# Kernel tuning notes

Hardware: AMD Instinct MI355X
Metric: run time of the kernel (lower is better)

Reference implementation:

```python
import jax, jax.numpy as jnp
import numpy as np

N = 50000
F = 128
E = 800000
HOP = 3
ALPHA = 0.2  # leaky relu slope


def setup_inputs() -> dict:
    key = jax.random.key(0)
    ks = jax.random.split(key, 6)
    x = jax.random.normal(ks[0], (N, F), dtype=jnp.float32)
    h0 = jax.random.normal(ks[1], (N, F), dtype=jnp.float32)
    edge_index = jax.random.randint(ks[2], (2, E), 0, N, dtype=jnp.int32)
    edge_weight = jax.random.uniform(ks[3], (E,), dtype=jnp.float32)
    # xavier-uniform-ish params
    lim_w = float(np.sqrt(6.0 / (F + F)))
    W_att = jax.random.uniform(ks[4], (F, F), dtype=jnp.float32, minval=-lim_w, maxval=lim_w)
    lim_a = 1.414 * float(np.sqrt(6.0 / (2 * F + 1)))
    a = jax.random.uniform(ks[5], (2 * F, 1), dtype=jnp.float32, minval=-lim_a, maxval=lim_a)
    temp = jnp.zeros((4,), dtype=jnp.float32)
    return {"x": x, "h0": h0, "edge_index": edge_index, "edge_weight": edge_weight,
            "W_att": W_att, "a": a, "temp": temp}


def _segment_softmax(e, rows, num_segments):
    m = jax.ops.segment_max(e, rows, num_segments=num_segments)
    m = jnp.where(jnp.isfinite(m), m, 0.0)  # guard empty rows
    ex = jnp.exp(e - m[rows])
    s = jax.ops.segment_sum(ex, rows, num_segments=num_segments)
    s = jnp.where(s > 0, s, 1.0)
    return ex / s[rows]


def reference(x, h0, edge_index, edge_weight, W_att, a, temp):
    rows, cols = edge_index[0], edge_index[1]
    # --- attention (edge-wise, never materializing dense NxN e) ---
    feat = x @ W_att                       # [N, F]
    f1 = (feat @ a[:F]).squeeze(-1)        # [N]
    f2 = (feat @ a[F:]).squeeze(-1)        # [N]
    e = f1[rows] + f2[cols]                # e[i,j] at edges
    e = jnp.where(e > 0, e, ALPHA * e)     # leaky relu
    att = _segment_softmax(e, rows, N)     # sparse row softmax values
    P = 0.5 * att
    # --- lifting bases ---
    coe = jax.nn.sigmoid(temp)
    rowsum = jax.ops.segment_sum(edge_weight * P, rows, num_segments=N)  # [N]
    update = x
    feat_prime = None
    for step in range(HOP):
        # sparse mm: U @ update
        update = jax.ops.segment_sum(att[:, None] * update[cols], rows, num_segments=N)
        feat_even = coe[0] * x + update
        feat_odd = update - feat_even * rowsum[:, None]
        feat_prime = feat_odd if step == 0 else coe[2] * feat_prime + (1.0 - coe[2]) * feat_odd
    return feat_prime
```

## Files before the change

kernel.cpp:

```cpp
#include <hip/hip_runtime.h>
#include <hip/hip_fp16.h>

#define NN 50000
#define FF 128
#define EE 800000
#define ALPHA 0.2f
#define ESHIFT 4.0f

#define NBINS 196
#define CAPB 5120
#define EPB 2048
#define NWIN 784
#define WCAP 1600

__global__ void k_w(const float* __restrict__ W, const float* __restrict__ a,
                    float* __restrict__ w12) {
    int k = threadIdx.x;
    float s1 = 0.f, s2 = 0.f;
    const float* wr = W + k * FF;
    for (int j = 0; j < FF; ++j) {
        float w = wr[j];
        s1 += w * a[j];
        s2 += w * a[FF + j];
    }
    w12[k] = s1;
    w12[FF + k] = s2;
}

__global__ void k_f(const float* __restrict__ x, const float* __restrict__ w12,
                    float* __restrict__ f1, float* __restrict__ f2,
                    __half* __restrict__ xh) {
    int gid = blockIdx.x * blockDim.x + threadIdx.x;
    int node = gid >> 6;
    int lane = threadIdx.x & 63;
    if (node >= NN) return;
    float2 xv = ((const float2*)(x + (size_t)node * FF))[lane];
    ((__half2*)(xh + (size_t)node * FF))[lane] = __float22half2_rn(xv);
    float2 w1 = ((const float2*)w12)[lane];
    float2 w2 = ((const float2*)(w12 + FF))[lane];
    float s1 = xv.x * w1.x + xv.y * w1.y;
    float s2 = xv.x * w2.x + xv.y * w2.y;
#pragma unroll
    for (int o = 32; o > 0; o >>= 1) {
        s1 += __shfl_down(s1, o);
        s2 += __shfl_down(s2, o);
    }
    if (lane == 0) { f1[node] = s1; f2[node] = s2; }
}

__global__ void k_bin(const int* __restrict__ rows, const int* __restrict__ cols,
                      const float* __restrict__ ew, const float* __restrict__ f1,
                      const float* __restrict__ f2, int* __restrict__ bin_fill,
                      int2* __restrict__ binbuf) {
    __shared__ int cnt[NBINS];
    __shared__ int gbase[NBINS];
    int tid = threadIdx.x;
    if (tid < NBINS) cnt[tid] = 0;
    __syncthreads();
    int e0 = blockIdx.x * EPB;
    int rk[8], bn[8], rc[8], pay[8];
    bool vl[8];
#pragma unroll
    for (int k = 0; k < 8; ++k) {
        int e = e0 + k * 256 + tid;
        vl[k] = e < EE;
        if (vl[k]) {
            int r = rows[e], c = cols[e];
            float v = f1[r] + f2[c];
            v = v > 0.f ? v : ALPHA * v;
            float ex = __expf(v - ESHIFT);
            union { int i; __half2 h; } p;
            p.h = __floats2half2_rn(ex, ew[e] * ex);
            pay[k] = p.i;
            rc[k] = (r << 16) | c;
            bn[k] = r >> 8;
            rk[k] = atomicAdd(&cnt[bn[k]], 1);
        }
    }
    __syncthreads();
    if (tid < NBINS) {
        int c0 = cnt[tid];
        gbase[tid] = c0 ? atomicAdd(&bin_fill[tid], c0) : 0;
    }
    __syncthreads();
#pragma unroll
    for (int k = 0; k < 8; ++k) {
        if (vl[k]) {
            int pos = gbase[bn[k]] + rk[k];
            if (pos < CAPB) binbuf[(size_t)bn[k] * CAPB + pos] = make_int2(rc[k], pay[k]);
        }
    }
}

__global__ void k_csr(const int* __restrict__ bin_fill, const int2* __restrict__ binbuf,
                      int2* __restrict__ csr, int2* __restrict__ rowinfo) {
    __shared__ int lfill[64];
    __shared__ int pbase[65];
    __shared__ int cursor[64];
    int tid = threadIdx.x;
    int w = blockIdx.x;
    int bin = w >> 2, q = w & 3;
    int cnt = bin_fill[bin];
    if (cnt > CAPB) cnt = CAPB;
    if (tid < 64) lfill[tid] = 0;
    __syncthreads();
    const int2* bb = binbuf + (size_t)bin * CAPB;
    for (int i = tid; i < cnt; i += 256) {
        int rl = (bb[i].x >> 16) & 0xFF;
        if ((rl >> 6) == q) atomicAdd(&lfill[rl & 63], 1);
    }
    __syncthreads();
    if (tid < 64) {
        int pc = (lfill[tid] + 3) & ~3;
        int s = pc;
#pragma unroll
        for (int o = 1; o < 64; o <<= 1) {
            int t = __shfl_up(s, o);
            if (tid >= o) s += t;
        }
        pbase[tid + 1] = s;
        if (tid == 0) pbase[0] = 0;
    }
    __syncthreads();
    int wbase = w * WCAP;
    if (tid < 64) cursor[tid] = wbase + pbase[tid];
    __syncthreads();
    for (int i = tid; i < cnt; i += 256) {
        int2 e = bb[i];
        int rl = (e.x >> 16) & 0xFF;
        if ((rl >> 6) == q) {
            int p = atomicAdd(&cursor[rl & 63], 1);
            csr[p] = make_int2(e.x & 0xFFFF, e.y);
        }
    }
    __syncthreads();
    if (tid < 64) {
        int r = (bin << 8) + (q << 6) + tid;
        if (r < NN) {
            int beg = wbase + pbase[tid];
            int dreal = lfill[tid];
            int dpad = (dreal + 3) & ~3;
            for (int t = dreal; t < dpad; ++t) csr[beg + t] = make_int2(0, 0);
            rowinfo[r] = make_int2(beg, dpad);
        }
    }
}

__global__ void k_hop(const float* __restrict__ x, const __half* __restrict__ uin,
                      __half* __restrict__ uout, const int2* __restrict__ rowinfo,
                      const int2* __restrict__ csr, const float* __restrict__ temp,
                      __half* __restrict__ S, float* __restrict__ out, int step) {
    int wave = threadIdx.x >> 6;
    int lane = threadIdx.x & 63;
    int r = __builtin_amdgcn_readfirstlane(blockIdx.x * 4 + wave);
    if (r >= NN) return;
    int2 ri = rowinfo[r];
    const unsigned long long* bk = (const unsigned long long*)(csr + ri.x);
    int d = ri.y;
    int s = lane >> 4;
    int fl = lane & 15;
    float ax[8];
#pragma unroll
    for (int k = 0; k < 8; ++k) ax[k] = 0.f;
    float se = 0.f, sw = 0.f;
    int j = 0;
    for (; j + 16 <= d; j += 16) {
        unsigned long long b[4];
        uint4 h[4];
#pragma unroll
        for (int g = 0; g < 4; ++g)
            b[g] = __builtin_nontemporal_load(bk + j + 4 * g + s);
#pragma unroll
        for (int g = 0; g < 4; ++g) {
            int col = (int)(unsigned)(b[g] & 0xFFFFFFFFull);
            h[g] = ((const uint4*)(uin + (size_t)col * FF))[fl];
        }
#pragma unroll
        for (int g = 0; g < 4; ++g) {
            union { unsigned u; __half2 h2; } p;
            p.u = (unsigned)(b[g] >> 32);
            float2 ee = __half22float2(p.h2);
            se += ee.x;
            sw += ee.y;
            const __half2* hh = (const __half2*)&h[g];
#pragma unroll
            for (int t = 0; t < 4; ++t) {
                float2 u2 = __half22float2(hh[t]);
                ax[2 * t] += ee.x * u2.x;
                ax[2 * t + 1] += ee.x * u2.y;
            }
        }
    }
    for (; j < d; j += 4) {
        unsigned long long b = __builtin_nontemporal_load(bk + j + s);
        int col = (int)(unsigned)(b & 0xFFFFFFFFull);
        uint4 h = ((const uint4*)(uin + (size_t)col * FF))[fl];
        union { unsigned u; __half2 h2; } p;
        p.u = (unsigned)(b >> 32);
        float2 ee = __half22float2(p.h2);
        se += ee.x;
        sw += ee.y;
        const __half2* hh = (const __half2*)&h;
#pragma unroll
        for (int t = 0; t < 4; ++t) {
            float2 u2 = __half22float2(hh[t]);
            ax[2 * t] += ee.x * u2.x;
            ax[2 * t + 1] += ee.x * u2.y;
        }
    }
#pragma unroll
    for (int o = 16; o < 64; o <<= 1) {
#pragma unroll
        for (int k = 0; k < 8; ++k) ax[k] += __shfl_xor(ax[k], o);
        se += __shfl_xor(se, o);
        sw += __shfl_xor(sw, o);
    }
    float inv = se > 0.f ? 1.f / se : 0.f;
#pragma unroll
    for (int k = 0; k < 8; ++k) ax[k] *= inv;
    float c2 = 1.f / (1.f + __expf(-temp[2]));
    uint4* Sr = (uint4*)(S + (size_t)r * FF);
    if (step == 0) {
        if (s == 0) {
            union { uint4 u; __half2 h2[4]; } o1, o2;
            float w0 = c2 * c2;
#pragma unroll
            for (int t = 0; t < 4; ++t) {
                o1.h2[t] = __floats2half2_rn(ax[2 * t], ax[2 * t + 1]);
                o2.h2[t] = __floats2half2_rn(w0 * ax[2 * t], w0 * ax[2 * t + 1]);
            }
            ((uint4*)(uout + (size_t)r * FF))[fl] = o1.u;
            Sr[fl] = o2.u;
        }
    } else if (step == 1) {
        if (s == 0) {
            float w1 = c2 * (1.f - c2);
            union { uint4 u; __half2 h2[4]; } o1, sv;
            sv.u = Sr[fl];
#pragma unroll
            for (int t = 0; t < 4; ++t) {
                o1.h2[t] = __floats2half2_rn(ax[2 * t], ax[2 * t + 1]);
                float2 svf = __half22float2(sv.h2[t]);
                sv.h2[t] = __floats2half2_rn(svf.x + w1 * ax[2 * t],
                                             svf.y + w1 * ax[2 * t + 1]);
            }
            ((uint4*)(uout + (size_t)r * FF))[fl] = o1.u;
            Sr[fl] = sv.u;
        }
    } else {
        if (s == 0) {
            float rs = 0.5f * sw * inv;
            float coe0 = 1.f / (1.f + __expf(-temp[0]));
            float w2 = 1.f - c2;
            float k1 = 1.f - rs, k2 = coe0 * rs;
            union { uint4 u; __half2 h2[4]; } sv;
            sv.u = Sr[fl];
            const float4* xr = (const float4*)(x + (size_t)r * FF);
            float4* orow = (float4*)(out + (size_t)r * FF);
            float4 xv0 = xr[2 * fl], xv1 = xr[2 * fl + 1];
            float res[8];
#pragma unroll
            for (int t = 0; t < 4; ++t) {
                float2 svf = __half22float2(sv.h2[t]);
                res[2 * t] = k1 * (svf.x + w2 * ax[2 * t]);
                res[2 * t + 1] = k1 * (svf.y + w2 * ax[2 * t + 1]);
            }
            orow[2 * fl] = make_float4(res[0] - k2 * xv0.x, res[1] - k2 * xv0.y,
                                       res[2] - k2 * xv0.z, res[3] - k2 * xv0.w);
            orow[2 * fl + 1] = make_float4(res[4] - k2 * xv1.x, res[5] - k2 * xv1.y,
                                           res[6] - k2 * xv1.z, res[7] - k2 * xv1.w);
        }
    }
}

extern "C" void kernel_launch(void* const* d_in, const int* in_sizes, int n_in,
                              void* d_out, int out_size, void* d_ws, size_t ws_size,
                              hipStream_t stream) {
    const float* x = (const float*)d_in[0];
    const int* eidx = (const int*)d_in[2];
    const int* rows = eidx;
    const int* cols = eidx + EE;
    const float* ew = (const float*)d_in[3];
    const float* W = (const float*)d_in[4];
    const float* a = (const float*)d_in[5];
    const float* temp = (const float*)d_in[6];
    float* out = (float*)d_out;

    float* ws = (float*)d_ws;
    int* bin_fill = (int*)ws;
    float* w12 = ws + 256;
    float* f1 = ws + 512;
    float* f2 = f1 + NN;
    int2* rowinfo = (int2*)(f2 + NN);
    int2* csr = rowinfo + NN;
    __half* xh = (__half*)(csr + (size_t)NWIN * WCAP);
    __half* uh0 = xh + (size_t)NN * FF;
    __half* Sb = uh0 + (size_t)NN * FF;
    int2* binbuf = (int2*)Sb;
    __half* uh1 = xh;

    hipMemsetAsync(bin_fill, 0, NBINS * sizeof(int), stream);

    k_w<<<1, 128, 0, stream>>>(W, a, w12);
    k_f<<<(NN + 3) / 4, 256, 0, stream>>>(x, w12, f1, f2, xh);
    k_bin<<<(EE + EPB - 1) / EPB, 256, 0, stream>>>(rows, cols, ew, f1, f2, bin_fill, binbuf);
    k_csr<<<NWIN, 256, 0, stream>>>(bin_fill, binbuf, csr, rowinfo);
    k_hop<<<(NN + 3) / 4, 256, 0, stream>>>(x, xh, uh0, rowinfo, csr, temp, Sb, out, 0);
    k_hop<<<(NN + 3) / 4, 256, 0, stream>>>(x, uh0, uh1, rowinfo, csr, temp, Sb, out, 1);
    k_hop<<<(NN + 3) / 4, 256, 0, stream>>>(x, uh1, nullptr, rowinfo, csr, temp, Sb, out, 2);
}
```

Baseline: 248.9 us.

## Pre-normalize attention into packed 4-byte CSR and process two rows per wave

k_csr now computes per-row softmax sums once. It packs each edge as a 16-bit column plus a half-precision normalized attention weight, and stores the row sum of weighted attention in a separate array. This halves the CSR bytes streamed in each of the three hop kernels and removes the repeated edge-weight sum. k_hop now handles two rows per wave (r and r+N/2) to raise memory-level parallelism. The costs are guarded per-element loads, work imbalance from iterating to the larger of the two degrees, and a serial per-row pass in k_csr.

```diff
diff --git a/kernel.cpp b/kernel.cpp
--- a/kernel.cpp
+++ b/kernel.cpp
@@ -2,6 +2,7 @@
 #include <hip/hip_fp16.h>
 
 #define NN 50000
+#define HALFN 25000
 #define FF 128
 #define EE 800000
 #define ALPHA 0.2f
@@ -12,6 +13,9 @@
 #define EPB 2048
 #define NWIN 784
 #define WCAP 1600
+
+union H2 { unsigned u; int i; __half2 h; };
+union G4 { uint4 u; __half2 h2[4]; };
 
 __global__ void k_w(const float* __restrict__ W, const float* __restrict__ a,
                     float* __restrict__ w12) {
@@ -69,7 +73,7 @@
             float v = f1[r] + f2[c];
             v = v > 0.f ? v : ALPHA * v;
             float ex = __expf(v - ESHIFT);
-            union { int i; __half2 h; } p;
+            H2 p;
             p.h = __floats2half2_rn(ex, ew[e] * ex);
             pay[k] = p.i;
             rc[k] = (r << 16) | c;
@@ -93,7 +97,8 @@
 }
 
 __global__ void k_csr(const int* __restrict__ bin_fill, const int2* __restrict__ binbuf,
-                      int2* __restrict__ csr, int2* __restrict__ rowinfo) {
+                      int2* __restrict__ csr, unsigned* __restrict__ csr2,
+                      int2* __restrict__ rowinfo, float* __restrict__ rs) {
     __shared__ int lfill[64];
     __shared__ int pbase[65];
     __shared__ int cursor[64];
@@ -140,136 +145,157 @@
             int beg = wbase + pbase[tid];
             int dreal = lfill[tid];
             int dpad = (dreal + 3) & ~3;
-            for (int t = dreal; t < dpad; ++t) csr[beg + t] = make_int2(0, 0);
+            float se = 0.f, sw = 0.f;
+            for (int i = 0; i < dreal; ++i) {
+                H2 pu;
+                pu.i = csr[beg + i].y;
+                float2 f = __half22float2(pu.h);
+                se += f.x;
+                sw += f.y;
+            }
+            float inv = se > 0.f ? 1.f / se : 0.f;
+            rs[r] = 0.5f * sw * inv;
+            for (int i = 0; i < dreal; ++i) {
+                int2 e = csr[beg + i];
+                H2 pu;
+                pu.i = e.y;
+                float att = __half22float2(pu.h).x * inv;
+                unsigned ab = (unsigned)__half_as_ushort(__float2half_rn(att));
+                csr2[beg + i] = (unsigned)e.x | (ab << 16);
+            }
+            for (int i = dreal; i < dpad; ++i) csr2[beg + i] = 0u;
             rowinfo[r] = make_int2(beg, dpad);
         }
     }
 }
 
-__global__ void k_hop(const float* __restrict__ x, const __half* __restrict__ uin,
-                      __half* __restrict__ uout, const int2* __restrict__ rowinfo,
-                      const int2* __restrict__ csr, const float* __restrict__ temp,
-                      __half* __restrict__ S, float* __restrict__ out, int step) {
+__device__ __forceinline__ void emit_row(
+    int step, int r, int fl, const float* ax, float se,
+    __half* __restrict__ uout, __half* __restrict__ S, const float* __restrict__ rs,
+    const float* __restrict__ x, float* __restrict__ out,
+    float w0, float w1c, float w2c, float coe0)
+{
+    float inv = se > 0.f ? 1.f / se : 0.f;
+    float a[8];
+#pragma unroll
+    for (int k = 0; k < 8; ++k) a[k] = ax[k] * inv;
+    if (step == 0) {
+        G4 o1, o2;
+#pragma unroll
+        for (int t = 0; t < 4; ++t) {
+            o1.h2[t] = __floats2half2_rn(a[2 * t], a[2 * t + 1]);
+            o2.h2[t] = __floats2half2_rn(w0 * a[2 * t], w0 * a[2 * t + 1]);
+        }
+        ((uint4*)(uout + (size_t)r * FF))[fl] = o1.u;
+        ((uint4*)(S + (size_t)r * FF))[fl] = o2.u;
+    } else if (step == 1) {
+        G4 o1, sv;
+        sv.u = ((const uint4*)(S + (size_t)r * FF))[fl];
+#pragma unroll
+        for (int t = 0; t < 4; ++t) {
+            o1.h2[t] = __floats2half2_rn(a[2 * t], a[2 * t + 1]);
+            float2 svf = __half22float2(sv.h2[t]);
+            sv.h2[t] = __floats2half2_rn(svf.x + w1c * a[2 * t],
+                                         svf.y + w1c * a[2 * t + 1]);
+        }
+        ((uint4*)(uout + (size_t)r * FF))[fl] = o1.u;
+        ((uint4*)(S + (size_t)r * FF))[fl] = sv.u;
+    } else {
+        float rsv = rs[r];
+        float k1 = 1.f - rsv, k2 = coe0 * rsv;
+        G4 sv;
+        sv.u = ((const uint4*)(S + (size_t)r * FF))[fl];
+        const float4* xr = (const float4*)(x + (size_t)r * FF);
+        float4* orow = (float4*)(out + (size_t)r * FF);
+        float4 xv0 = xr[2 * fl], xv1 = xr[2 * fl + 1];
+        float res[8];
+#pragma unroll
+        for (int t = 0; t < 4; ++t) {
+            float2 svf = __half22float2(sv.h2[t]);
+            res[2 * t] = k1 * (svf.x + w2c * a[2 * t]);
+            res[2 * t + 1] = k1 * (svf.y + w2c * a[2 * t + 1]);
+        }
+        orow[2 * fl] = make_float4(res[0] - k2 * xv0.x, res[1] - k2 * xv0.y,
+                                   res[2] - k2 * xv0.z, res[3] - k2 * xv0.w);
+        orow[2 * fl + 1] = make_float4(res[4] - k2 * xv1.x, res[5] - k2 * xv1.y,
+                                       res[6] - k2 * xv1.z, res[7] - k2 * xv1.w);
+    }
+}
+
+__global__ __launch_bounds__(256) void k_hop(
+    const float* __restrict__ x, const __half* __restrict__ uin,
+    __half* __restrict__ uout, const int2* __restrict__ rowinfo,
+    const unsigned* __restrict__ csr2, const float* __restrict__ temp,
+    const float* __restrict__ rs, __half* __restrict__ S,
+    float* __restrict__ out, int step)
+{
     int wave = threadIdx.x >> 6;
     int lane = threadIdx.x & 63;
-    int r = __builtin_amdgcn_readfirstlane(blockIdx.x * 4 + wave);
-    if (r >= NN) return;
-    int2 ri = rowinfo[r];
-    const unsigned long long* bk = (const unsigned long long*)(csr + ri.x);
-    int d = ri.y;
+    int w = blockIdx.x * 4 + wave;
+    if (w >= HALFN) return;
     int s = lane >> 4;
     int fl = lane & 15;
-    float ax[8];
-#pragma unroll
-    for (int k = 0; k < 8; ++k) ax[k] = 0.f;
-    float se = 0.f, sw = 0.f;
-    int j = 0;
-    for (; j + 16 <= d; j += 16) {
-        unsigned long long b[4];
-        uint4 h[4];
-#pragma unroll
-        for (int g = 0; g < 4; ++g)
-            b[g] = __builtin_nontemporal_load(bk + j + 4 * g + s);
+    int r0 = w, r1 = w + HALFN;
+    int2 ri0 = rowinfo[r0];
+    int2 ri1 = rowinfo[r1];
+    const unsigned* bk0 = csr2 + ri0.x;
+    const unsigned* bk1 = csr2 + ri1.x;
+    int d0 = ri0.y, d1 = ri1.y;
+    float ax0[8], ax1[8];
+#pragma unroll
+    for (int k = 0; k < 8; ++k) { ax0[k] = 0.f; ax1[k] = 0.f; }
+    float se0 = 0.f, se1 = 0.f;
+    int dmax = d0 > d1 ? d0 : d1;
+    for (int j = 0; j < dmax; j += 16) {
+        unsigned b0[4], b1[4];
+        G4 g0[4], g1[4];
 #pragma unroll
         for (int g = 0; g < 4; ++g) {
-            int col = (int)(unsigned)(b[g] & 0xFFFFFFFFull);
-            h[g] = ((const uint4*)(uin + (size_t)col * FF))[fl];
+            int e = j + 4 * g + s;
+            b0[g] = e < d0 ? bk0[e] : 0u;
+            b1[g] = e < d1 ? bk1[e] : 0u;
         }
 #pragma unroll
         for (int g = 0; g < 4; ++g) {
-            union { unsigned u; __half2 h2; } p;
-            p.u = (unsigned)(b[g] >> 32);
-            float2 ee = __half22float2(p.h2);
-            se += ee.x;
-            sw += ee.y;
-            const __half2* hh = (const __half2*)&h[g];
+            g0[g].u = make_uint4(0, 0, 0, 0);
+            if (b0[g]) g0[g].u = ((const uint4*)(uin + (size_t)(b0[g] & 0xFFFF) * FF))[fl];
+            g1[g].u = make_uint4(0, 0, 0, 0);
+            if (b1[g]) g1[g].u = ((const uint4*)(uin + (size_t)(b1[g] & 0xFFFF) * FF))[fl];
+        }
+#pragma unroll
+        for (int g = 0; g < 4; ++g) {
+            H2 p0, p1;
+            p0.u = b0[g] >> 16;
+            p1.u = b1[g] >> 16;
+            float at0 = __half22float2(p0.h).x;
+            float at1 = __half22float2(p1.h).x;
+            se0 += at0;
+            se1 += at1;
 #pragma unroll
             for (int t = 0; t < 4; ++t) {
-                float2 u2 = __half22float2(hh[t]);
-                ax[2 * t] += ee.x * u2.x;
-                ax[2 * t + 1] += ee.x * u2.y;
+                float2 u0 = __half22float2(g0[g].h2[t]);
+                float2 u1 = __half22float2(g1[g].h2[t]);
+                ax0[2 * t] += at0 * u0.x; ax0[2 * t + 1] += at0 * u0.y;
+                ax1[2 * t] += at1 * u1.x; ax1[2 * t + 1] += at1 * u1.y;
             }
         }
     }
-    for (; j < d; j += 4) {
-        unsigned long long b = __builtin_nontemporal_load(bk + j + s);
-        int col = (int)(unsigned)(b & 0xFFFFFFFFull);
-        uint4 h = ((const uint4*)(uin + (size_t)col * FF))[fl];
-        union { unsigned u; __half2 h2; } p;
-        p.u = (unsigned)(b >> 32);
-        float2 ee = __half22float2(p.h2);
-        se += ee.x;
-        sw += ee.y;
-        const __half2* hh = (const __half2*)&h;
-#pragma unroll
-        for (int t = 0; t < 4; ++t) {
-            float2 u2 = __half22float2(hh[t]);
-            ax[2 * t] += ee.x * u2.x;
-            ax[2 * t + 1] += ee.x * u2.y;
-        }
-    }
 #pragma unroll
     for (int o = 16; o < 64; o <<= 1) {
 #pragma unroll
-        for (int k = 0; k < 8; ++k) ax[k] += __shfl_xor(ax[k], o);
-        se += __shfl_xor(se, o);
-        sw += __shfl_xor(sw, o);
-    }
-    float inv = se > 0.f ? 1.f / se : 0.f;
-#pragma unroll
-    for (int k = 0; k < 8; ++k) ax[k] *= inv;
-    float c2 = 1.f / (1.f + __expf(-temp[2]));
-    uint4* Sr = (uint4*)(S + (size_t)r * FF);
-    if (step == 0) {
-        if (s == 0) {
-            union { uint4 u; __half2 h2[4]; } o1, o2;
-            float w0 = c2 * c2;
-#pragma unroll
-            for (int t = 0; t < 4; ++t) {
-                o1.h2[t] = __floats2half2_rn(ax[2 * t], ax[2 * t + 1]);
-                o2.h2[t] = __floats2half2_rn(w0 * ax[2 * t], w0 * ax[2 * t + 1]);
-            }
-            ((uint4*)(uout + (size_t)r * FF))[fl] = o1.u;
-            Sr[fl] = o2.u;
-        }
-    } else if (step == 1) {
-        if (s == 0) {
-            float w1 = c2 * (1.f - c2);
-            union { uint4 u; __half2 h2[4]; } o1, sv;
-            sv.u = Sr[fl];
-#pragma unroll
-            for (int t = 0; t < 4; ++t) {
-                o1.h2[t] = __floats2half2_rn(ax[2 * t], ax[2 * t + 1]);
-                float2 svf = __half22float2(sv.h2[t]);
-                sv.h2[t] = __floats2half2_rn(svf.x + w1 * ax[2 * t],
-                                             svf.y + w1 * ax[2 * t + 1]);
-            }
-            ((uint4*)(uout + (size_t)r * FF))[fl] = o1.u;
-            Sr[fl] = sv.u;
-        }
-    } else {
-        if (s == 0) {
-            float rs = 0.5f * sw * inv;
-            float coe0 = 1.f / (1.f + __expf(-temp[0]));
-            float w2 = 1.f - c2;
-            float k1 = 1.f - rs, k2 = coe0 * rs;
-            union { uint4 u; __half2 h2[4]; } sv;
-            sv.u = Sr[fl];
-            const float4* xr = (const float4*)(x + (size_t)r * FF);
-            float4* orow = (float4*)(out + (size_t)r * FF);
-            float4 xv0 = xr[2 * fl], xv1 = xr[2 * fl + 1];
-            float res[8];
-#pragma unroll
-            for (int t = 0; t < 4; ++t) {
-                float2 svf = __half22float2(sv.h2[t]);
-                res[2 * t] = k1 * (svf.x + w2 * ax[2 * t]);
-                res[2 * t + 1] = k1 * (svf.y + w2 * ax[2 * t + 1]);
-            }
-            orow[2 * fl] = make_float4(res[0] - k2 * xv0.x, res[1] - k2 * xv0.y,
-                                       res[2] - k2 * xv0.z, res[3] - k2 * xv0.w);
-            orow[2 * fl + 1] = make_float4(res[4] - k2 * xv1.x, res[5] - k2 * xv1.y,
-                                           res[6] - k2 * xv1.z, res[7] - k2 * xv1.w);
-        }
+        for (int k = 0; k < 8; ++k) {
+            ax0[k] += __shfl_xor(ax0[k], o);
+            ax1[k] += __shfl_xor(ax1[k], o);
+        }
+        se0 += __shfl_xor(se0, o);
+        se1 += __shfl_xor(se1, o);
+    }
+    if (s == 0) {
+        float c2 = 1.f / (1.f + __expf(-temp[2]));
+        float coe0 = 1.f / (1.f + __expf(-temp[0]));
+        float w0 = c2 * c2, w1c = c2 * (1.f - c2), w2c = 1.f - c2;
+        emit_row(step, r0, fl, ax0, se0, uout, S, rs, x, out, w0, w1c, w2c, coe0);
+        emit_row(step, r1, fl, ax1, se1, uout, S, rs, x, out, w0, w1c, w2c, coe0);
     }
 }
 
@@ -291,21 +317,23 @@
     float* w12 = ws + 256;
     float* f1 = ws + 512;
     float* f2 = f1 + NN;
-    int2* rowinfo = (int2*)(f2 + NN);
+    float* rs = f2 + NN;
+    int2* rowinfo = (int2*)(rs + NN);
     int2* csr = rowinfo + NN;
-    __half* xh = (__half*)(csr + (size_t)NWIN * WCAP);
+    unsigned* csr2 = (unsigned*)(csr + (size_t)NWIN * WCAP);
+    __half* xh = (__half*)(csr2 + (size_t)NWIN * WCAP);
     __half* uh0 = xh + (size_t)NN * FF;
     __half* Sb = uh0 + (size_t)NN * FF;
     int2* binbuf = (int2*)Sb;
     __half* uh1 = xh;
 
-    hipMemsetAsync(bin_fill, 0, NBINS * sizeof(int), stream);
+    (void)hipMemsetAsync(bin_fill, 0, NBINS * sizeof(int), stream);
 
     k_w<<<1, 128, 0, stream>>>(W, a, w12);
     k_f<<<(NN + 3) / 4, 256, 0, stream>>>(x, w12, f1, f2, xh);
     k_bin<<<(EE + EPB - 1) / EPB, 256, 0, stream>>>(rows, cols, ew, f1, f2, bin_fill, binbuf);
-    k_csr<<<NWIN, 256, 0, stream>>>(bin_fill, binbuf, csr, rowinfo);
-    k_hop<<<(NN + 3) / 4, 256, 0, stream>>>(x, xh, uh0, rowinfo, csr, temp, Sb, out, 0);
-    k_hop<<<(NN + 3) / 4, 256, 0, stream>>>(x, uh0, uh1, rowinfo, csr, temp, Sb, out, 1);
-    k_hop<<<(NN + 3) / 4, 256, 0, stream>>>(x, uh1, nullptr, rowinfo, csr, temp, Sb, out, 2);
-}
+    k_csr<<<NWIN, 256, 0, stream>>>(bin_fill, binbuf, csr, csr2, rowinfo, rs);
+    k_hop<<<HALFN / 4, 256, 0, stream>>>(x, xh, uh0, rowinfo, csr2, temp, rs, Sb, out, 0);
+    k_hop<<<HALFN / 4, 256, 0, stream>>>(x, uh0, uh1, rowinfo, csr2, temp, rs, Sb, out, 1);
+    k_hop<<<HALFN / 4, 256, 0, stream>>>(x, uh1, uh0, rowinfo, csr2, temp, rs, Sb, out, 2);
+}
```

New measurement: 280.2 us. 1.13x slower.
